# Kernel tuning notes

Hardware: AMD Instinct MI355X
Metric: run time of the kernel (lower is better)

## Reference

```python
import jax, jax.numpy as jnp
import numpy as np

H, QK, VD = 16, 64, 64  # n_heads, qk_dim, v_dim

def _feature_map(t):
    # elu(x) + 1, the standard positive feature map for linear attention
    return jax.nn.elu(t) + 1.0

def setup_inputs() -> dict:
    key = jax.random.key(0)
    ks = jax.random.split(key, 5)
    B, T, D = 2, 4096, 1024
    s = 0.02
    return {
        "x": jax.random.normal(ks[0], (B, T, D), dtype=jnp.float32),
        "WQ": jax.random.normal(ks[1], (H * QK, D), dtype=jnp.float32) * s,
        "WK": jax.random.normal(ks[2], (H * QK, D), dtype=jnp.float32) * s,
        "WV": jax.random.normal(ks[3], (H * VD, D), dtype=jnp.float32) * s,
        "Wproj": jax.random.normal(ks[4], (D, VD), dtype=jnp.float32) * s,
        "start_pos": 0,
    }

def reference(x, WQ, WK, WV, Wproj, start_pos):
    B, T, D = x.shape
    # QKV projections (no bias), reshape to heads
    q = (x @ WQ.T).reshape(B, T, H, QK)
    k = (x @ WK.T).reshape(B, T, H, QK)
    v = (x @ WV.T).reshape(B, T, H, VD)
    q = _feature_map(q)
    k = _feature_map(k)
    # global key-value summary per head: [B,H,QK,VD]
    kv = jnp.einsum('bthd,bthm->bhdm', k, v)
    # normalizer: q . sum_t(k)
    z = 1.0 / jnp.einsum('bthd,bhd->bth', q, k.sum(axis=1))
    o = jnp.einsum('bthd,bhdm->bthm', q, kv) * z[..., None]  # [B,T,H,VD]
    # per-head output projection (module applies Linear(v_dim, dim) on last axis)
    return jnp.einsum('bthm,cm->bthc', o, Wproj)  # [B,T,H,D]
```

## Files before the change

kernel.cpp:

```cpp
#include <hip/hip_runtime.h>

#define Bb 2
#define Tt 4096
#define Dd 1024
#define Hh 16
#define QKd 64
#define VDd 64
#define BT (Bb*Tt)
#define NCH 16
#define CHUNK (Tt/NCH)

#define OFF_QF  0
#define OFF_KF  (OFF_QF + (size_t)BT*Dd)
#define OFF_V   (OFF_KF + (size_t)BT*Dd)
#define OFF_KVP (OFF_V + (size_t)BT*Dd)
#define OFF_KSP (OFF_KVP + (size_t)NCH*32*4096)
#define OFF_KV  (OFF_KSP + (size_t)NCH*32*64)
#define OFF_KS  (OFF_KV + (size_t)32*4096)
#define OFF_XA  (OFF_KS + (size_t)32*64)
#define OFF_WB  (OFF_XA + (size_t)BT*512)
#define OFF_KVQB (OFF_WB + (size_t)3072*512)
#define OFF_QSB (OFF_KVQB + (size_t)32*1024*32)

typedef __attribute__((ext_vector_type(8))) short short8;
typedef __attribute__((ext_vector_type(4))) float f32x4;

__device__ __forceinline__ float featmap(float x) {
    return x > 0.f ? x + 1.f : __expf(x);
}

__device__ __forceinline__ unsigned short bf16_rne(float f) {
    unsigned int u = __float_as_uint(f);
    unsigned int r = u + 0x7fffu + ((u >> 16) & 1u);
    return (unsigned short)(r >> 16);
}

__global__ __launch_bounds__(256) void cast_a(const float* __restrict__ src,
                                              unsigned short* __restrict__ dst)
{
    int idx = blockIdx.x * 256 + threadIdx.x;
    int m = idx >> 8;
    int c = (idx & 255) << 2;
    float4 v = *(const float4*)&src[(size_t)m * 1024 + c];
    ushort4 o;
    o.x = bf16_rne(v.x); o.y = bf16_rne(v.y); o.z = bf16_rne(v.z); o.w = bf16_rne(v.w);
    *(ushort4*)&dst[(size_t)m * 1024 + c] = o;
}

__global__ __launch_bounds__(256) void cast_w3(const float* __restrict__ WQ,
                                               const float* __restrict__ WK,
                                               const float* __restrict__ WV,
                                               unsigned short* __restrict__ dst)
{
    int idx = blockIdx.x * 256 + threadIdx.x;
    int w = idx >> 18;
    int r = idx & 262143;
    const float* src = (w == 0) ? WQ : ((w == 1) ? WK : WV);
    int m = r >> 8;
    int c = (r & 255) << 2;
    float4 v = *(const float4*)&src[(size_t)m * 1024 + c];
    ushort4 o;
    o.x = bf16_rne(v.x); o.y = bf16_rne(v.y); o.z = bf16_rne(v.z); o.w = bf16_rne(v.w);
    *(ushort4*)&dst[(size_t)(w*1024 + m) * 1024 + c] = o;
}

#define GLLDS(gp, lp) __builtin_amdgcn_global_load_lds( \
    (const __attribute__((address_space(1))) void*)(gp), \
    (__attribute__((address_space(3))) void*)(lp), 16, 0, 0)

__global__ __launch_bounds__(512, 2) void gemm_qkv(const unsigned short* __restrict__ A,
                                                   const unsigned short* __restrict__ W,
                                                   float* __restrict__ qf,
                                                   float* __restrict__ kf,
                                                   float* __restrict__ vf)
{
    extern __shared__ unsigned short lds[];
    const int tid  = threadIdx.x;
    const int lane = tid & 63;
    const int wave = tid >> 6;
    const int wm = (wave >> 2) * 128;
    const int wn = (wave & 3) * 64;
    const int bid = blockIdx.x;
    const int nb = (bid & 7) * 48 + (bid >> 3);
    const int mblk = nb / 12, nblk = nb % 12;
    const int m0 = mblk * 256, n0 = nblk * 256;

    f32x4 acc[8][4] = {};

    auto stage = [&](int buf, int kt) {
        const int k0 = kt * 64;
        unsigned short* ab = &lds[buf * 32768];
        unsigned short* bb = ab + 16384;
        #pragma unroll
        for (int i = 0; i < 4; ++i) {
            int s = i * 512 + tid;
            int row = s >> 3, g = s & 7;
            int gl = g ^ (row & 7);
            GLLDS(&A[(size_t)(m0 + row) * 1024 + k0 + gl * 8], &ab[s * 8]);
        }
        #pragma unroll
        for (int i = 0; i < 4; ++i) {
            int s = i * 512 + tid;
            int row = s >> 3, g = s & 7;
            int gl = g ^ (row & 7);
            GLLDS(&W[(size_t)(n0 + row) * 1024 + k0 + gl * 8], &bb[s * 8]);
        }
    };

    stage(0, 0);
    for (int kt = 0; kt < 16; ++kt) {
        const int buf = kt & 1;
        if (kt + 1 < 16) {
            stage(buf ^ 1, kt + 1);
            asm volatile("s_waitcnt vmcnt(8)" ::: "memory");
        } else {
            asm volatile("s_waitcnt vmcnt(0)" ::: "memory");
        }
        __builtin_amdgcn_s_barrier();
        __builtin_amdgcn_sched_barrier(0);
        const unsigned short* ab = &lds[buf * 32768];
        const unsigned short* bb = ab + 16384;
        #pragma unroll
        for (int ks = 0; ks < 2; ++ks) {
            short8 af[8], bf2[4];
            #pragma unroll
            for (int mi = 0; mi < 8; ++mi) {
                int row = wm + mi * 16 + (lane & 15);
                int g = ks * 4 + (lane >> 4);
                af[mi] = *(const short8*)&ab[row * 64 + (g ^ (row & 7)) * 8];
            }
            #pragma unroll
            for (int ni = 0; ni < 4; ++ni) {
                int row = wn + ni * 16 + (lane & 15);
                int g = ks * 4 + (lane >> 4);
                bf2[ni] = *(const short8*)&bb[row * 64 + (g ^ (row & 7)) * 8];
            }
            __builtin_amdgcn_s_setprio(1);
            #pragma unroll
            for (int mi = 0; mi < 8; ++mi)
                #pragma unroll
                for (int ni = 0; ni < 4; ++ni)
                    acc[mi][ni] = __builtin_amdgcn_mfma_f32_16x16x32_bf16(af[mi], bf2[ni], acc[mi][ni], 0, 0, 0);
            __builtin_amdgcn_s_setprio(0);
        }
        __builtin_amdgcn_s_barrier();
        __builtin_amdgcn_sched_barrier(0);
    }

    float* Cb = (n0 < 1024) ? qf : ((n0 < 2048) ? kf : vf);
    const int elu = (n0 < 2048);
    const int c0 = n0 & 1023;
    #pragma unroll
    for (int mi = 0; mi < 8; ++mi) {
        #pragma unroll
        for (int ni = 0; ni < 4; ++ni) {
            #pragma unroll
            for (int r = 0; r < 4; ++r) {
                float v = acc[mi][ni][r];
                if (elu) v = featmap(v);
                int row = m0 + wm + mi*16 + ((lane >> 4) << 2) + r;
                int col = c0 + wn + ni*16 + (lane & 15);
                Cb[(size_t)row * 1024 + col] = v;
            }
        }
    }
}

__global__ __launch_bounds__(256) void kv_partial(const float* __restrict__ kf,
        const float* __restrict__ vf, float* __restrict__ kvpart, float* __restrict__ kspart)
{
    const int bh = blockIdx.x;
    const int ch = blockIdx.y;
    const int b = bh >> 4, h = bh & 15;
    __shared__ float sk[8][64];
    __shared__ float sv[8][64];
    const int tid = threadIdx.x;
    const int r0 = (tid >> 4) << 2;
    const int c0 = (tid & 15) << 2;
    const int tt = tid >> 5;
    const int rem = tid & 31;
    const int which = rem >> 4;
    const int d4 = (rem & 15) << 2;
    const float* src = which ? vf : kf;
    float acc[4][4] = {};
    float ksl = 0.f;
    for (int t0 = ch * CHUNK; t0 < (ch + 1) * CHUNK; t0 += 8) {
        const int t = t0 + tt;
        float4 val = *(const float4*)&src[(size_t)(b*Tt + t)*Dd + h*QKd + d4];
        __syncthreads();
        if (which) *(float4*)&sv[tt][d4] = val;
        else       *(float4*)&sk[tt][d4] = val;
        __syncthreads();
        #pragma unroll
        for (int s = 0; s < 8; ++s) {
            float4 k4v = *(const float4*)&sk[s][r0];
            float4 v4v = *(const float4*)&sv[s][c0];
            float kvv[4] = {k4v.x,k4v.y,k4v.z,k4v.w};
            float vvv[4] = {v4v.x,v4v.y,v4v.z,v4v.w};
            #pragma unroll
            for (int i = 0; i < 4; ++i)
                #pragma unroll
                for (int j = 0; j < 4; ++j)
                    acc[i][j] = fmaf(kvv[i], vvv[j], acc[i][j]);
        }
        if (tid < 64) {
            #pragma unroll
            for (int s = 0; s < 8; ++s) ksl += sk[s][tid];
        }
    }
    const size_t base = (size_t)(ch*32 + bh) * 4096;
    #pragma unroll
    for (int i = 0; i < 4; ++i) {
        float4 o = {acc[i][0], acc[i][1], acc[i][2], acc[i][3]};
        *(float4*)&kvpart[base + (r0+i)*64 + c0] = o;
    }
    if (tid < 64) kspart[(size_t)(ch*32 + bh)*64 + tid] = ksl;
}

__global__ __launch_bounds__(256) void kv_reduce(const float* __restrict__ kvpart,
        const float* __restrict__ kspart, float* __restrict__ kv, float* __restrict__ ksum)
{
    int g = blockIdx.x * 256 + threadIdx.x;
    if (g < 32*4096) {
        float s = 0.f;
        #pragma unroll
        for (int c = 0; c < NCH; ++c) s += kvpart[(size_t)c*(32*4096) + g];
        kv[g] = s;
    } else if (g < 32*4096 + 32*64) {
        int g2 = g - 32*4096;
        float s = 0.f;
        #pragma unroll
        for (int c = 0; c < NCH; ++c) s += kspart[(size_t)c*(32*64) + g2];
        ksum[g2] = s;
    }
}

__global__ __launch_bounds__(256) void kvpb_kernel(const float* __restrict__ kv,
        const float* __restrict__ wproj, unsigned short* __restrict__ kvqb)
{
    int flat = blockIdx.x * 256 + threadIdx.x;
    int d = flat & 63;
    int c = (flat >> 6) & 1023;
    int bh = flat >> 16;
    const float4* kr = (const float4*)&kv[(size_t)(bh*64 + d)*64];
    const float4* wr = (const float4*)&wproj[(size_t)c*64];
    float s = 0.f;
    #pragma unroll
    for (int m = 0; m < 16; ++m) {
        float4 a = kr[m], bq = wr[m];
        s += a.x*bq.x + a.y*bq.y + a.z*bq.z + a.w*bq.w;
    }
    kvqb[((size_t)bh*1024 + c) * 64 + d] = bf16_rne(s);
}

__global__ __launch_bounds__(256) void zq_kernel(const float* __restrict__ qf,
        const float* __restrict__ ksum, unsigned short* __restrict__ qsb)
{
    int row = blockIdx.x * 16 + (threadIdx.x >> 4);
    int l16 = threadIdx.x & 15;
    int bt = row >> 4, h = row & 15;
    int b = bt >> 12, t = bt & 4095;
    float4 qv = *(const float4*)&qf[(size_t)bt*1024 + h*64 + l16*4];
    float4 kq = *(const float4*)&ksum[(size_t)(b*16 + h)*64 + l16*4];
    float p = qv.x*kq.x + qv.y*kq.y + qv.z*kq.z + qv.w*kq.w;
    p += __shfl_xor(p, 1); p += __shfl_xor(p, 2);
    p += __shfl_xor(p, 4); p += __shfl_xor(p, 8);
    float zv = 1.f / p;
    ushort4 o;
    o.x = bf16_rne(qv.x*zv); o.y = bf16_rne(qv.y*zv);
    o.z = bf16_rne(qv.z*zv); o.w = bf16_rne(qv.w*zv);
    *(ushort4*)&qsb[(((size_t)(b*16 + h)*4096 + t) << 6) + l16*4] = o;
}

__global__ __launch_bounds__(256) void fgemm(const unsigned short* __restrict__ qsb,
        const unsigned short* __restrict__ kvqb, float* __restrict__ out)
{
    __shared__ unsigned short Als[2][128*32];
    __shared__ unsigned short Bls[2][128*32];
    const int tid  = threadIdx.x;
    const int lane = tid & 63;
    const int wave = tid >> 6;
    const int bh = blockIdx.z;
    const int b = bh >> 4, h = bh & 15;
    const int t0 = blockIdx.y * 128;
    const int c0 = blockIdx.x * 128;
    const int wr = (wave >> 1) * 64;
    const int wc = (wave & 1) * 64;
    f32x4 acc[4][4] = {};

    auto stage = [&](int buf, int kt) {
        const int k0 = kt * 32;
        #pragma unroll
        for (int i = 0; i < 2; ++i) {
            int s = i * 256 + tid;
            int row = s >> 2, g = s & 3;
            GLLDS(&qsb[((size_t)bh*4096 + t0 + row) * 64 + k0 + g * 8], &Als[buf][s * 8]);
            GLLDS(&kvqb[((size_t)bh*1024 + c0 + row) * 64 + k0 + g * 8], &Bls[buf][s * 8]);
        }
    };

    stage(0, 0);
    const int arow = (lane & 15) * 32 + (lane >> 4) * 8;
    for (int kt = 0; kt < 2; ++kt) {
        const int buf = kt & 1;
        __syncthreads();
        if (kt + 1 < 2) stage(buf ^ 1, kt + 1);
        short8 af[4], bfr[4];
        #pragma unroll
        for (int m = 0; m < 4; ++m)
            af[m] = *(const short8*)&Als[buf][(wr + m*16)*32 + arow];
        #pragma unroll
        for (int n = 0; n < 4; ++n)
            bfr[n] = *(const short8*)&Bls[buf][(wc + n*16)*32 + arow];
        #pragma unroll
        for (int m = 0; m < 4; ++m)
            #pragma unroll
            for (int n = 0; n < 4; ++n)
                acc[m][n] = __builtin_amdgcn_mfma_f32_16x16x32_bf16(af[m], bfr[n], acc[m][n], 0, 0, 0);
    }

    #pragma unroll
    for (int m = 0; m < 4; ++m) {
        #pragma unroll
        for (int n = 0; n < 4; ++n) {
            #pragma unroll
            for (int r = 0; r < 4; ++r) {
                int trow = t0 + wr + m*16 + ((lane >> 4) << 2) + r;
                int col = c0 + wc + n*16 + (lane & 15);
                out[((size_t)(b*4096 + trow)*16 + h)*1024 + col] = acc[m][n][r];
            }
        }
    }
}

extern "C" void kernel_launch(void* const* d_in, const int* in_sizes, int n_in,
                              void* d_out, int out_size, void* d_ws, size_t ws_size,
                              hipStream_t stream)
{
    const float* x  = (const float*)d_in[0];
    const float* WQ = (const float*)d_in[1];
    const float* WK = (const float*)d_in[2];
    const float* WV = (const float*)d_in[3];
    const float* Wp = (const float*)d_in[4];
    float* ws = (float*)d_ws;
    float* qf     = ws + OFF_QF;
    float* kf     = ws + OFF_KF;
    float* vf     = ws + OFF_V;
    float* kvpart = ws + OFF_KVP;
    float* kspart = ws + OFF_KSP;
    float* kv     = ws + OFF_KV;
    float* ksum   = ws + OFF_KS;
    unsigned short* xa   = (unsigned short*)(ws + OFF_XA);
    unsigned short* wb   = (unsigned short*)(ws + OFF_WB);
    unsigned short* kvqb = (unsigned short*)(ws + OFF_KVQB);
    unsigned short* qsb  = (unsigned short*)(ws + OFF_QSB);
    float* out = (float*)d_out;

    (void)hipFuncSetAttribute((const void*)gemm_qkv,
                              hipFuncAttributeMaxDynamicSharedMemorySize, 131072);

    dim3 blk(256);
    cast_a<<<(BT*1024/4)/256, blk, 0, stream>>>(x, xa);
    cast_w3<<<(3*1024*1024/4)/256, blk, 0, stream>>>(WQ, WK, WV, wb);
    gemm_qkv<<<384, 512, 131072, stream>>>(xa, wb, qf, kf, vf);
    kv_partial<<<dim3(32, NCH), blk, 0, stream>>>(kf, vf, kvpart, kspart);
    kv_reduce<<<(32*4096 + 32*64 + 255)/256, blk, 0, stream>>>(kvpart, kspart, kv, ksum);
    kvpb_kernel<<<(32*1024*64)/256, blk, 0, stream>>>(kv, Wp, kvqb);
    zq_kernel<<<(BT*Hh)/16, blk, 0, stream>>>(qf, ksum, qsb);
    fgemm<<<dim3(8, 32, 32), blk, 0, stream>>>(qsb, kvqb, out);
}
```

Baseline: 320.9 us.

## Store feature-mapped Q as bf16 and apply normalizer in final GEMM epilogue

```diff
diff --git a/kernel.cpp b/kernel.cpp
--- a/kernel.cpp
+++ b/kernel.cpp
@@ -10,17 +10,17 @@
 #define NCH 16
 #define CHUNK (Tt/NCH)
 
-#define OFF_QF  0
-#define OFF_KF  (OFF_QF + (size_t)BT*Dd)
+#define OFF_KF  0
 #define OFF_V   (OFF_KF + (size_t)BT*Dd)
 #define OFF_KVP (OFF_V + (size_t)BT*Dd)
 #define OFF_KSP (OFF_KVP + (size_t)NCH*32*4096)
 #define OFF_KV  (OFF_KSP + (size_t)NCH*32*64)
 #define OFF_KS  (OFF_KV + (size_t)32*4096)
-#define OFF_XA  (OFF_KS + (size_t)32*64)
+#define OFF_Z   (OFF_KS + (size_t)32*64)
+#define OFF_QB  (OFF_Z + (size_t)BT*Hh)
+#define OFF_XA  (OFF_QB + (size_t)BT*512)
 #define OFF_WB  (OFF_XA + (size_t)BT*512)
 #define OFF_KVQB (OFF_WB + (size_t)3072*512)
-#define OFF_QSB (OFF_KVQB + (size_t)32*1024*32)
 
 typedef __attribute__((ext_vector_type(8))) short short8;
 typedef __attribute__((ext_vector_type(4))) float f32x4;
@@ -33,6 +33,9 @@
     unsigned int u = __float_as_uint(f);
     unsigned int r = u + 0x7fffu + ((u >> 16) & 1u);
     return (unsigned short)(r >> 16);
+}
+__device__ __forceinline__ float bf16_to_f(unsigned short h) {
+    return __uint_as_float(((unsigned int)h) << 16);
 }
 
 __global__ __launch_bounds__(256) void cast_a(const float* __restrict__ src,
@@ -70,7 +73,7 @@
 
 __global__ __launch_bounds__(512, 2) void gemm_qkv(const unsigned short* __restrict__ A,
                                                    const unsigned short* __restrict__ W,
-                                                   float* __restrict__ qf,
+                                                   unsigned short* __restrict__ qb16,
                                                    float* __restrict__ kf,
                                                    float* __restrict__ vf)
 {
@@ -78,18 +81,18 @@
     const int tid  = threadIdx.x;
     const int lane = tid & 63;
     const int wave = tid >> 6;
-    const int wm = (wave >> 2) * 128;
-    const int wn = (wave & 3) * 64;
+    const int wm = (wave >> 1) * 64;
+    const int wn = (wave & 1) * 64;
     const int bid = blockIdx.x;
-    const int nb = (bid & 7) * 48 + (bid >> 3);
-    const int mblk = nb / 12, nblk = nb % 12;
-    const int m0 = mblk * 256, n0 = nblk * 256;
-
-    f32x4 acc[8][4] = {};
+    const int nb = (bid & 7) * 96 + (bid >> 3);
+    const int mblk = nb / 24, nblk = nb % 24;
+    const int m0 = mblk * 256, n0 = nblk * 128;
+
+    f32x4 acc[4][4] = {};
 
     auto stage = [&](int buf, int kt) {
         const int k0 = kt * 64;
-        unsigned short* ab = &lds[buf * 32768];
+        unsigned short* ab = &lds[buf * 24576];
         unsigned short* bb = ab + 16384;
         #pragma unroll
         for (int i = 0; i < 4; ++i) {
@@ -99,7 +102,7 @@
             GLLDS(&A[(size_t)(m0 + row) * 1024 + k0 + gl * 8], &ab[s * 8]);
         }
         #pragma unroll
-        for (int i = 0; i < 4; ++i) {
+        for (int i = 0; i < 2; ++i) {
             int s = i * 512 + tid;
             int row = s >> 3, g = s & 7;
             int gl = g ^ (row & 7);
@@ -112,19 +115,19 @@
         const int buf = kt & 1;
         if (kt + 1 < 16) {
             stage(buf ^ 1, kt + 1);
-            asm volatile("s_waitcnt vmcnt(8)" ::: "memory");
+            asm volatile("s_waitcnt vmcnt(6)" ::: "memory");
         } else {
             asm volatile("s_waitcnt vmcnt(0)" ::: "memory");
         }
         __builtin_amdgcn_s_barrier();
         __builtin_amdgcn_sched_barrier(0);
-        const unsigned short* ab = &lds[buf * 32768];
+        const unsigned short* ab = &lds[buf * 24576];
         const unsigned short* bb = ab + 16384;
         #pragma unroll
         for (int ks = 0; ks < 2; ++ks) {
-            short8 af[8], bf2[4];
-            #pragma unroll
-            for (int mi = 0; mi < 8; ++mi) {
+            short8 af[4], bf2[4];
+            #pragma unroll
+            for (int mi = 0; mi < 4; ++mi) {
                 int row = wm + mi * 16 + (lane & 15);
                 int g = ks * 4 + (lane >> 4);
                 af[mi] = *(const short8*)&ab[row * 64 + (g ^ (row & 7)) * 8];
@@ -137,7 +140,7 @@
             }
             __builtin_amdgcn_s_setprio(1);
             #pragma unroll
-            for (int mi = 0; mi < 8; ++mi)
+            for (int mi = 0; mi < 4; ++mi)
                 #pragma unroll
                 for (int ni = 0; ni < 4; ++ni)
                     acc[mi][ni] = __builtin_amdgcn_mfma_f32_16x16x32_bf16(af[mi], bf2[ni], acc[mi][ni], 0, 0, 0);
@@ -147,20 +150,23 @@
         __builtin_amdgcn_sched_barrier(0);
     }
 
-    float* Cb = (n0 < 1024) ? qf : ((n0 < 2048) ? kf : vf);
-    const int elu = (n0 < 2048);
     const int c0 = n0 & 1023;
     #pragma unroll
-    for (int mi = 0; mi < 8; ++mi) {
+    for (int mi = 0; mi < 4; ++mi) {
         #pragma unroll
         for (int ni = 0; ni < 4; ++ni) {
             #pragma unroll
             for (int r = 0; r < 4; ++r) {
                 float v = acc[mi][ni][r];
-                if (elu) v = featmap(v);
                 int row = m0 + wm + mi*16 + ((lane >> 4) << 2) + r;
                 int col = c0 + wn + ni*16 + (lane & 15);
-                Cb[(size_t)row * 1024 + col] = v;
+                if (nblk < 8) {
+                    qb16[(size_t)row * 1024 + col] = bf16_rne(featmap(v));
+                } else if (nblk < 16) {
+                    kf[(size_t)row * 1024 + col] = featmap(v);
+                } else {
+                    vf[(size_t)row * 1024 + col] = v;
+                }
             }
         }
     }
@@ -253,30 +259,29 @@
     kvqb[((size_t)bh*1024 + c) * 64 + d] = bf16_rne(s);
 }
 
-__global__ __launch_bounds__(256) void zq_kernel(const float* __restrict__ qf,
-        const float* __restrict__ ksum, unsigned short* __restrict__ qsb)
+__global__ __launch_bounds__(256) void z_kernel(const unsigned short* __restrict__ qb16,
+        const float* __restrict__ ksum, float* __restrict__ z)
 {
     int row = blockIdx.x * 16 + (threadIdx.x >> 4);
     int l16 = threadIdx.x & 15;
     int bt = row >> 4, h = row & 15;
-    int b = bt >> 12, t = bt & 4095;
-    float4 qv = *(const float4*)&qf[(size_t)bt*1024 + h*64 + l16*4];
+    int b = bt >> 12;
+    ushort4 qu = *(const ushort4*)&qb16[(size_t)bt*1024 + h*64 + l16*4];
     float4 kq = *(const float4*)&ksum[(size_t)(b*16 + h)*64 + l16*4];
-    float p = qv.x*kq.x + qv.y*kq.y + qv.z*kq.z + qv.w*kq.w;
+    float p = bf16_to_f(qu.x)*kq.x + bf16_to_f(qu.y)*kq.y
+            + bf16_to_f(qu.z)*kq.z + bf16_to_f(qu.w)*kq.w;
     p += __shfl_xor(p, 1); p += __shfl_xor(p, 2);
     p += __shfl_xor(p, 4); p += __shfl_xor(p, 8);
-    float zv = 1.f / p;
-    ushort4 o;
-    o.x = bf16_rne(qv.x*zv); o.y = bf16_rne(qv.y*zv);
-    o.z = bf16_rne(qv.z*zv); o.w = bf16_rne(qv.w*zv);
-    *(ushort4*)&qsb[(((size_t)(b*16 + h)*4096 + t) << 6) + l16*4] = o;
-}
-
-__global__ __launch_bounds__(256) void fgemm(const unsigned short* __restrict__ qsb,
-        const unsigned short* __restrict__ kvqb, float* __restrict__ out)
+    if (l16 == 0) z[row] = 1.f / p;
+}
+
+__global__ __launch_bounds__(256) void fgemm(const unsigned short* __restrict__ qb16,
+        const unsigned short* __restrict__ kvqb, const float* __restrict__ z,
+        float* __restrict__ out)
 {
     __shared__ unsigned short Als[2][128*32];
     __shared__ unsigned short Bls[2][128*32];
+    __shared__ float zs[128];
     const int tid  = threadIdx.x;
     const int lane = tid & 63;
     const int wave = tid >> 6;
@@ -288,13 +293,15 @@
     const int wc = (wave & 1) * 64;
     f32x4 acc[4][4] = {};
 
+    if (tid < 128) zs[tid] = z[(size_t)(b*4096 + t0 + tid)*16 + h];
+
     auto stage = [&](int buf, int kt) {
         const int k0 = kt * 32;
         #pragma unroll
         for (int i = 0; i < 2; ++i) {
             int s = i * 256 + tid;
             int row = s >> 2, g = s & 3;
-            GLLDS(&qsb[((size_t)bh*4096 + t0 + row) * 64 + k0 + g * 8], &Als[buf][s * 8]);
+            GLLDS(&qb16[((size_t)(b*4096) + t0 + row) * 1024 + h*64 + k0 + g * 8], &Als[buf][s * 8]);
             GLLDS(&kvqb[((size_t)bh*1024 + c0 + row) * 64 + k0 + g * 8], &Bls[buf][s * 8]);
         }
     };
@@ -325,9 +332,10 @@
         for (int n = 0; n < 4; ++n) {
             #pragma unroll
             for (int r = 0; r < 4; ++r) {
-                int trow = t0 + wr + m*16 + ((lane >> 4) << 2) + r;
+                int rowl = wr + m*16 + ((lane >> 4) << 2) + r;
+                int trow = t0 + rowl;
                 int col = c0 + wc + n*16 + (lane & 15);
-                out[((size_t)(b*4096 + trow)*16 + h)*1024 + col] = acc[m][n][r];
+                out[((size_t)(b*4096 + trow)*16 + h)*1024 + col] = acc[m][n][r] * zs[rowl];
             }
         }
     }
@@ -343,29 +351,29 @@
     const float* WV = (const float*)d_in[3];
     const float* Wp = (const float*)d_in[4];
     float* ws = (float*)d_ws;
-    float* qf     = ws + OFF_QF;
     float* kf     = ws + OFF_KF;
     float* vf     = ws + OFF_V;
     float* kvpart = ws + OFF_KVP;
     float* kspart = ws + OFF_KSP;
     float* kv     = ws + OFF_KV;
     float* ksum   = ws + OFF_KS;
+    float* zz     = ws + OFF_Z;
+    unsigned short* qb16 = (unsigned short*)(ws + OFF_QB);
     unsigned short* xa   = (unsigned short*)(ws + OFF_XA);
     unsigned short* wb   = (unsigned short*)(ws + OFF_WB);
     unsigned short* kvqb = (unsigned short*)(ws + OFF_KVQB);
-    unsigned short* qsb  = (unsigned short*)(ws + OFF_QSB);
     float* out = (float*)d_out;
 
     (void)hipFuncSetAttribute((const void*)gemm_qkv,
-                              hipFuncAttributeMaxDynamicSharedMemorySize, 131072);
+                              hipFuncAttributeMaxDynamicSharedMemorySize, 98304);
 
     dim3 blk(256);
     cast_a<<<(BT*1024/4)/256, blk, 0, stream>>>(x, xa);
     cast_w3<<<(3*1024*1024/4)/256, blk, 0, stream>>>(WQ, WK, WV, wb);
-    gemm_qkv<<<384, 512, 131072, stream>>>(xa, wb, qf, kf, vf);
+    gemm_qkv<<<768, 512, 98304, stream>>>(xa, wb, qb16, kf, vf);
     kv_partial<<<dim3(32, NCH), blk, 0, stream>>>(kf, vf, kvpart, kspart);
     kv_reduce<<<(32*4096 + 32*64 + 255)/256, blk, 0, stream>>>(kvpart, kspart, kv, ksum);
     kvpb_kernel<<<(32*1024*64)/256, blk, 0, stream>>>(kv, Wp, kvqb);
-    zq_kernel<<<(BT*Hh)/16, blk, 0, stream>>>(qf, ksum, qsb);
-    fgemm<<<dim3(8, 32, 32), blk, 0, stream>>>(qsb, kvqb, out);
-}
+    z_kernel<<<(BT*Hh)/16, blk, 0, stream>>>(qb16, ksum, zz);
+    fgemm<<<dim3(8, 32, 32), blk, 0, stream>>>(qb16, kvqb, zz, out);
+}
```

Result: slower. 367.2 us (+14.4%).
